# Kernel optimization log

Measured on AMD Instinct MI355X. Metric: run time of the kernel, lower is better.

## Reference

```python
import math
import jax, jax.numpy as jnp
import numpy as np

I_DIM = 64
N_MODES = 16
FACTOR = 4
EPS = 1e-5


def group_norm(x, w, b):
    # x: [B, M, N, C] channels-last; torch GroupNorm(C//16, C) over (group_channels, M, N)
    B, M, N, C = x.shape
    g = C // 16
    xr = x.reshape(B, M, N, g, C // g)
    mean = xr.mean(axis=(1, 2, 4), keepdims=True)
    var = xr.var(axis=(1, 2, 4), keepdims=True)
    xr = (xr - mean) * jax.lax.rsqrt(var + EPS)
    return xr.reshape(B, M, N, C) * w + b


def feed_forward(x, res, l1w, l1b, l2w, l2b, g1w, g1b, g2w, g2b, g3w, g3b):
    h = x @ l1w + l1b                      # [B,M,N,C*factor]
    h = group_norm(h, g1w, g1b)            # fork_1
    h = jax.nn.relu(h)
    h = h @ l2w + l2b                      # [B,M,N,C]
    h = group_norm(h, g2w, g2b)            # fork_2
    h = res + h
    h = group_norm(h, g3w, g3b)            # fork_3
    return h


def setup_inputs() -> dict:
    key = jax.random.key(0)
    ks = jax.random.split(key, 20)
    B, M, N, I = 4, 128, 128, I_DIM
    H = I * FACTOR
    z = jax.random.normal(ks[0], (B, 2 * M * N * I, 1), dtype=jnp.float32)
    x = jax.random.normal(ks[1], (B, M * N * I, 1), dtype=jnp.float32)
    # fourier weights [in, out, nm, nm, 2], xavier-ish scale
    fw_scale = math.sqrt(2.0 / (I + I))
    fw1 = jax.random.normal(ks[2], (I, I, N_MODES, N_MODES, 2), dtype=jnp.float32) * fw_scale
    fw2 = jax.random.normal(ks[3], (I, I, N_MODES, N_MODES, 2), dtype=jnp.float32) * fw_scale
    def ff_params(k0):
        kk = jax.random.split(k0, 4)
        return dict(
            l1w=jax.random.normal(kk[0], (I, H), dtype=jnp.float32) * math.sqrt(2.0 / (I + H)),
            l1b=jnp.zeros((H,), jnp.float32),
            l2w=jax.random.normal(kk[1], (H, I), dtype=jnp.float32) * math.sqrt(2.0 / (I + H)),
            l2b=jnp.zeros((I,), jnp.float32),
            g1w=jnp.ones((H,), jnp.float32), g1b=jnp.zeros((H,), jnp.float32),
            g2w=jnp.ones((I,), jnp.float32), g2b=jnp.zeros((I,), jnp.float32),
            g3w=jnp.ones((I,), jnp.float32), g3b=jnp.zeros((I,), jnp.float32),
        )
    bp = ff_params(ks[4])
    fp = ff_params(ks[5])
    out = {"z": z, "x": x, "fw1": fw1, "fw2": fw2}
    for name, p in (("b", bp), ("f", fp)):
        for k, v in p.items():
            out[f"{name}_{k}"] = v
    return out


def reference(z, x, fw1, fw2,
              b_l1w, b_l1b, b_l2w, b_l2b, b_g1w, b_g1b, b_g2w, b_g2b, b_g3w, b_g3b,
              f_l1w, f_l1b, f_l2w, f_l2b, f_g1w, f_g1b, f_g2w, f_g2b, f_g3w, f_g3b):
    I = I_DIM
    nm = N_MODES
    B = x.shape[0]
    M = N = int(math.sqrt(x.shape[1] // I))
    x4 = x.reshape(B, M, N, I)
    z5 = z.reshape(B, 2, M, N, I)
    backcast, forecast = z5[:, 0], z5[:, 1]
    x4 = x4 - backcast
    xc = jnp.transpose(x4, (0, 3, 1, 2))          # [B, I, M, N]
    x_ft = jnp.fft.rfft2(xc, s=(M, N), norm='ortho')  # [B, I, M, N//2+1] complex64
    w1 = fw1[..., 0] + 1j * fw1[..., 1]
    w2 = fw2[..., 0] + 1j * fw2[..., 1]
    top = jnp.einsum('bixy,ioxy->boxy', x_ft[:, :, :nm, :nm], w1)
    bot = jnp.einsum('bixy,ioxy->boxy', x_ft[:, :, -nm:, :nm], w2)
    out_ft = jnp.zeros((B, I, N, M // 2 + 1), dtype=x_ft.dtype)
    out_ft = out_ft.at[:, :, :nm, :nm].set(top).at[:, :, -nm:, :nm].set(bot)
    xo = jnp.fft.irfft2(out_ft, s=(N, M), norm='ortho')  # [B, I, M, N]
    xo = jnp.transpose(xo, (0, 2, 3, 1))                  # [B, M, N, I]
    backcast = feed_forward(xo, backcast, b_l1w, b_l1b, b_l2w, b_l2b,
                            b_g1w, b_g1b, b_g2w, b_g2b, b_g3w, b_g3b)
    forecast = feed_forward(xo, forecast, f_l1w, f_l1b, f_l2w, f_l2b,
                            f_g1w, f_g1b, f_g2w, f_g2b, f_g3w, f_g3b)
    out = jnp.stack([backcast, forecast], axis=1)         # [B, 2, M, N, I]
    return out.reshape(B, 2 * M * N * I, 1)
```

## Files before the change

kernel.cpp:

```cpp
#include <hip/hip_runtime.h>
#include <hip/hip_bf16.h>

typedef __hip_bfloat16 bf16;
typedef __attribute__((ext_vector_type(8))) short short8;
typedef __attribute__((ext_vector_type(4))) float f32x4;

#define PI2 6.283185307179586f
#define EPSV 1e-5f

__device__ __forceinline__ short f2bs(float f){
  bf16 h = __float2bfloat16(f);
  short s; __builtin_memcpy(&s, &h, 2); return s;
}
__device__ __forceinline__ float s2f(short s){
  bf16 h; __builtin_memcpy(&h, &s, 2); return __bfloat162float(h);
}
__device__ __forceinline__ float4 f4add(float4 a, float4 b){ return make_float4(a.x+b.x, a.y+b.y, a.z+b.z, a.w+b.w); }
__device__ __forceinline__ float4 f4sub(float4 a, float4 b){ return make_float4(a.x-b.x, a.y-b.y, a.z-b.z, a.w-b.w); }

__global__ __launch_bounds__(256) void k_prep(
    const float* __restrict__ fw1, const float* __restrict__ fw2,
    float2* __restrict__ FWT,
    const float* __restrict__ b_l1w, const float* __restrict__ b_l1b,
    const float* __restrict__ b_l2w, const float* __restrict__ b_l2b,
    const float* __restrict__ b_g1w, const float* __restrict__ b_g1b,
    const float* __restrict__ b_g2w, const float* __restrict__ b_g2b,
    const float* __restrict__ b_g3w, const float* __restrict__ b_g3b,
    const float* __restrict__ f_l1w, const float* __restrict__ f_l1b,
    const float* __restrict__ f_l2w, const float* __restrict__ f_l2b,
    const float* __restrict__ f_g1w, const float* __restrict__ f_g1b,
    const float* __restrict__ f_g2w, const float* __restrict__ f_g2b,
    const float* __restrict__ f_g3w, const float* __restrict__ f_g3b,
    short* __restrict__ W1g, short* __restrict__ W2g,
    float2* __restrict__ TWY, float2* __restrict__ TWX,
    float* __restrict__ PB, float* __restrict__ ST){
  __shared__ float Ls[16][512];
  int tid = threadIdx.x;
  if(blockIdx.x < 512){
    int arr = blockIdx.x >> 8, rem = blockIdx.x & 255;
    int i = rem >> 2, o0 = (rem & 3) * 16;
    const float* src = (arr ? fw2 : fw1) + ((size_t)(i*64 + o0))*512;
    for(int idx = tid; idx < 8192; idx += 256)
      Ls[idx >> 9][idx & 511] = src[idx];
    __syncthreads();
    int kxw = tid >> 4, ky = tid & 15;
    float2* dst = FWT + ((size_t)((arr*16 + kxw)*16 + ky))*4096 + i*64 + o0;
    for(int ol = 0; ol < 16; ol++)
      dst[ol] = make_float2(Ls[ol][tid*2], Ls[ol][tid*2 + 1]);
    return;
  }
  int i = (blockIdx.x - 512)*256 + tid;
  if(i < 32768){
    int br = i >> 14, r = i & 16383;
    int fid = r >> 9, lane = (r >> 3) & 63, e = r & 7;
    int hb = fid & 1, t = (fid >> 1) & 3, ch = fid >> 3;
    int l15 = lane & 15, quad = lane >> 4;
    int n = ch*64 + t*16 + l15;
    int k = hb*32 + quad*8 + e;
    const float* src = br ? f_l1w : b_l1w;
    W1g[i] = f2bs(src[k*256 + n]);
    return;
  }
  i -= 32768;
  if(i < 32768){
    int br = i >> 14, r = i & 16383;
    int fid = r >> 9, lane = (r >> 3) & 63, e = r & 7;
    int hb = fid & 1, t = (fid >> 1) & 3, ch = fid >> 3;
    int l15 = lane & 15, quad = lane >> 4;
    int n = t*16 + l15;
    int k = ch*64 + hb*32 + quad*8 + e;
    const float* src = br ? f_l2w : b_l2w;
    W2g[i] = f2bs(src[k*64 + n]);
    return;
  }
  i -= 32768;
  if(i < 2048){
    int ky = i >> 7, n = i & 127;
    float ang = PI2 * (float)((ky*n) & 127) / 128.0f;
    float s, c; sincosf(ang, &s, &c);
    TWY[i] = make_float2(c, s);
    return;
  }
  i -= 2048;
  if(i < 4096){
    int kp = i >> 7, m = i & 127;
    int kx = kp < 16 ? kp : 96 + kp;
    float ang = PI2 * (float)((kx*m) & 127) / 128.0f;
    float s, c; sincosf(ang, &s, &c);
    TWX[i] = make_float2(c, s);
    return;
  }
  i -= 4096;
  if(i < 384){ ST[i] = 0.f; return; }
  i -= 384;
  if(i < 2176){
    int br = i >= 1088; int o = i - br*1088;
    float* pb = PB + br*2048;
    float v;
    if(o < 256)       v = (br ? f_l1b : b_l1b)[o];
    else if(o < 512)  v = (br ? f_g1w : b_g1w)[o-256];
    else if(o < 768)  v = (br ? f_g1b : b_g1b)[o-512];
    else if(o < 832)  v = (br ? f_l2b : b_l2b)[o-768];
    else if(o < 896)  v = (br ? f_g2w : b_g2w)[o-832];
    else if(o < 960)  v = (br ? f_g2b : b_g2b)[o-896];
    else if(o < 1024) v = (br ? f_g3w : b_g3w)[o-960];
    else              v = (br ? f_g3b : b_g3b)[o-1024];
    pb[o] = v;
  }
}

__global__ __launch_bounds__(256) void k_ydft(const float* __restrict__ x,
                                              const float* __restrict__ z,
                                              const float2* __restrict__ TWY,
                                              float2* __restrict__ Y){
  __shared__ float P[32][64], Q[32][64], R[32][64], S[32][64];
  __shared__ float2 twl[16][32];
  int b = blockIdx.x >> 7, m = blockIdx.x & 127;
  int tid = threadIdx.x;
  const float4* xp = (const float4*)(x + ((size_t)(b*128 + m)*128)*64);
  const float4* zp = (const float4*)(z + ((size_t)((b*2 + 0)*128 + m)*128)*64);
  int i4 = tid & 15, n0 = tid >> 4;
  #pragma unroll
  for(int it = 0; it < 2; it++){
    int np = n0 + it*16;
    float4 ea = f4sub(xp[np*16 + i4],      zp[np*16 + i4]);
    float4 eb = f4sub(xp[(np+32)*16 + i4], zp[(np+32)*16 + i4]);
    float4 ec = f4sub(xp[(np+64)*16 + i4], zp[(np+64)*16 + i4]);
    float4 ed = f4sub(xp[(np+96)*16 + i4], zp[(np+96)*16 + i4]);
    float4 sum_ac = f4add(ea, ec), sum_bd = f4add(eb, ed);
    *(float4*)&P[np][i4*4] = f4add(sum_ac, sum_bd);
    *(float4*)&Q[np][i4*4] = f4sub(sum_ac, sum_bd);
    *(float4*)&R[np][i4*4] = f4sub(ea, ec);
    *(float4*)&S[np][i4*4] = f4sub(eb, ed);
  }
  for(int idx = tid; idx < 512; idx += 256)
    twl[idx >> 5][idx & 31] = TWY[(idx >> 5)*128 + (idx & 31)];
  __syncthreads();
  int i = tid & 63, kq = tid >> 6;
  float re[4] = {0,0,0,0}, im[4] = {0,0,0,0};
  for(int np = 0; np < 32; np++){
    float p = P[np][i], q = Q[np][i], r = R[np][i], s = S[np][i];
    float2 t0 = twl[kq*4 + 0][np];
    float2 t1 = twl[kq*4 + 1][np];
    float2 t2 = twl[kq*4 + 2][np];
    float2 t3 = twl[kq*4 + 3][np];
    re[0] += p*t0.x;            im[0] -= p*t0.y;
    re[1] += r*t1.x - s*t1.y;   im[1] -= s*t1.x + r*t1.y;
    re[2] += q*t2.x;            im[2] -= q*t2.y;
    re[3] += r*t3.x + s*t3.y;   im[3] += s*t3.x - r*t3.y;
  }
  #pragma unroll
  for(int j = 0; j < 4; j++)
    Y[((b*128 + m)*16 + kq*4 + j)*64 + i] = make_float2(re[j], im[j]);
}

__global__ __launch_bounds__(256) void k_xdft(const float2* __restrict__ Y,
                                              const float2* __restrict__ TWX,
                                              float2* __restrict__ X2){
  __shared__ float2 twl[16][64];
  __shared__ float sc[128][8];
  int bi = blockIdx.x;
  int b = bi >> 6, ky = (bi >> 2) & 15, half = (bi >> 1) & 1, ih = bi & 1;
  int tid = threadIdx.x;
  for(int idx = tid; idx < 1024; idx += 256)
    twl[idx >> 6][idx & 63] = TWX[(half*16 + (idx >> 6))*128 + (idx & 63)];
  __syncthreads();
  int i = ih*32 + (tid & 31), grp = (tid >> 5) & 3, mh2 = tid >> 7;
  const float2* yb = Y + (size_t)b*131072 + ky*64 + i;
  float re[4] = {0,0,0,0}, im[4] = {0,0,0,0};
  for(int mi = 0; mi < 32; mi++){
    int mp = mh2*32 + mi;
    float2 y1 = yb[(size_t)mp*1024];
    float2 y2 = yb[(size_t)(mp + 64)*1024];
    float2 ye = make_float2(y1.x + y2.x, y1.y + y2.y);
    float2 yo = make_float2(y1.x - y2.x, y1.y - y2.y);
    float2 t0 = twl[grp*4 + 0][mp];
    float2 t1 = twl[grp*4 + 1][mp];
    float2 t2 = twl[grp*4 + 2][mp];
    float2 t3 = twl[grp*4 + 3][mp];
    re[0] += ye.x*t0.x + ye.y*t0.y;  im[0] += ye.y*t0.x - ye.x*t0.y;
    re[1] += yo.x*t1.x + yo.y*t1.y;  im[1] += yo.y*t1.x - yo.x*t1.y;
    re[2] += ye.x*t2.x + ye.y*t2.y;  im[2] += ye.y*t2.x - ye.x*t2.y;
    re[3] += yo.x*t3.x + yo.y*t3.y;  im[3] += yo.y*t3.x - yo.x*t3.y;
  }
  if(mh2){
    int sl = tid & 127;
    #pragma unroll
    for(int j = 0; j < 4; j++){ sc[sl][j] = re[j]; sc[sl][4 + j] = im[j]; }
  }
  __syncthreads();
  if(!mh2){
    const float scn = 1.0f/128.0f;
    #pragma unroll
    for(int j = 0; j < 4; j++){
      float rr = (re[j] + sc[tid][j])*scn;
      float ii = (im[j] + sc[tid][4 + j])*scn;
      int kp = half*16 + grp*4 + j;
      X2[((b*32 + kp)*16 + ky)*64 + i] = make_float2(rr, ii);
    }
  }
}

__global__ __launch_bounds__(256) void k_mix(float2* __restrict__ X2,
                                             const float2* __restrict__ FWT){
  __shared__ float2 Xs[2][4][64];
  __shared__ float sc[2][64][8];
  int tid = threadIdx.x;
  for(int idx = tid; idx < 512; idx += 256){
    int pl = idx >> 8, b = (idx >> 6) & 3, i = idx & 63;
    int p = blockIdx.x*2 + pl; int kp = p >> 4, ky = p & 15;
    Xs[pl][b][i] = X2[((b*32 + kp)*16 + ky)*64 + i];
  }
  __syncthreads();
  int o = tid & 63, w = tid >> 6, pl = w >> 1, ih = w & 1;
  int p = blockIdx.x*2 + pl; int kp = p >> 4, ky = p & 15;
  int arr = kp < 16 ? 0 : 1, kxw = kp < 16 ? kp : kp - 16;
  const float2* wp = FWT + ((size_t)((arr*16 + kxw)*16 + ky))*4096;
  float rr[4] = {0,0,0,0}, ii[4] = {0,0,0,0};
  for(int i = ih*32; i < ih*32 + 32; i++){
    float2 wv = wp[i*64 + o];
    #pragma unroll
    for(int b = 0; b < 4; b++){
      float xr = Xs[pl][b][i].x, xi = Xs[pl][b][i].y;
      rr[b] += xr*wv.x - xi*wv.y;
      ii[b] += xr*wv.y + xi*wv.x;
    }
  }
  if(ih){
    #pragma unroll
    for(int b = 0; b < 4; b++){ sc[pl][o][b*2] = rr[b]; sc[pl][o][b*2 + 1] = ii[b]; }
  }
  __syncthreads();
  if(!ih){
    #pragma unroll
    for(int b = 0; b < 4; b++){
      float r2 = rr[b] + sc[pl][o][b*2], i2 = ii[b] + sc[pl][o][b*2 + 1];
      X2[((b*32 + kp)*16 + ky)*64 + o] = make_float2(r2, i2);
    }
  }
}

__global__ __launch_bounds__(256) void k_inv1(const float2* __restrict__ OF,
                                              const float2* __restrict__ TWX,
                                              float2* __restrict__ T){
  __shared__ float2 Fl[32][16];
  __shared__ float2 twl[32][64];
  int bi = blockIdx.x;
  int b = bi >> 6, ky = (bi >> 2) & 15, oq = bi & 3;
  int tid = threadIdx.x;
  for(int idx = tid; idx < 512; idx += 256){
    int kp = idx >> 4, ol = idx & 15;
    Fl[kp][ol] = OF[((b*32 + kp)*16 + ky)*64 + oq*16 + ol];
  }
  for(int idx = tid; idx < 2048; idx += 256){
    int kp = idx >> 6, ml = idx & 63;
    twl[kp][ml] = TWX[kp*128 + ml];
  }
  __syncthreads();
  int ol = tid & 15, mg = tid >> 4;
  float reE[4] = {0,0,0,0}, imE[4] = {0,0,0,0};
  float reO[4] = {0,0,0,0}, imO[4] = {0,0,0,0};
  for(int kp = 0; kp < 32; kp += 2){
    float2 fe = Fl[kp][ol], fo = Fl[kp + 1][ol];
    #pragma unroll
    for(int u = 0; u < 4; u++){
      float2 te = twl[kp][mg*4 + u], to = twl[kp + 1][mg*4 + u];
      reE[u] += fe.x*te.x - fe.y*te.y;
      imE[u] += fe.x*te.y + fe.y*te.x;
      reO[u] += fo.x*to.x - fo.y*to.y;
      imO[u] += fo.x*to.y + fo.y*to.x;
    }
  }
  int o = oq*16 + ol;
  #pragma unroll
  for(int u = 0; u < 4; u++){
    int ml = mg*4 + u;
    T[((b*128 + ml)*16 + ky)*64 + o]      = make_float2(reE[u] + reO[u], imE[u] + imO[u]);
    T[((b*128 + ml + 64)*16 + ky)*64 + o] = make_float2(reE[u] - reO[u], imE[u] - imO[u]);
  }
}

__global__ __launch_bounds__(256) void k_inv2(const float2* __restrict__ T,
                                              const float2* __restrict__ TWY,
                                              bf16* __restrict__ XO,
                                              float* __restrict__ CZ){
  __shared__ float2 twl[16][64];
  int b = blockIdx.x >> 6, mp = blockIdx.x & 63;
  int m0 = mp*2, m1 = m0 + 1;
  int tid = threadIdx.x;
  int flat = blockIdx.x*256 + tid;
  if(flat < 16640) CZ[flat] = 0.f;
  for(int idx = tid; idx < 1024; idx += 256)
    twl[idx >> 6][idx & 63] = TWY[(idx >> 6)*128 + (idx & 63)];
  int o = tid & 63, ng = tid >> 6;
  const float2* tp0 = T + ((size_t)(b*128 + m0)*16)*64 + o;
  const float2* tp1 = T + ((size_t)(b*128 + m1)*16)*64 + o;
  float t0a = tp0[0].x, t0b = tp1[0].x;
  float ax[15], ay[15], bx2[15], by2[15];
  #pragma unroll
  for(int u = 0; u < 15; u++){
    float2 v0 = tp0[(u + 1)*64]; ax[u]  = 2.f*v0.x; ay[u]  = 2.f*v0.y;
    float2 v1 = tp1[(u + 1)*64]; bx2[u] = 2.f*v1.x; by2[u] = 2.f*v1.y;
  }
  __syncthreads();
  const float scn = 1.0f/128.0f;
  bf16* xo0 = XO + ((size_t)(b*128 + m0)*128)*64 + o;
  bf16* xo1 = XO + ((size_t)(b*128 + m1)*128)*64 + o;
  for(int np = ng*16; np < ng*16 + 16; np++){
    float A0 = t0a, B0 = 0.f, A1 = t0b, B1 = 0.f;
    #pragma unroll
    for(int u = 0; u < 15; u++){
      float2 t = twl[u + 1][np];
      float pr0 = ax[u]*t.x  - ay[u]*t.y;
      float pr1 = bx2[u]*t.x - by2[u]*t.y;
      if(u & 1){ A0 += pr0; A1 += pr1; }
      else     { B0 += pr0; B1 += pr1; }
    }
    xo0[(size_t)np*64]        = __float2bfloat16((A0 + B0)*scn);
    xo0[(size_t)(np + 64)*64] = __float2bfloat16((A0 - B0)*scn);
    xo1[(size_t)np*64]        = __float2bfloat16((A1 + B1)*scn);
    xo1[(size_t)(np + 64)*64] = __float2bfloat16((A1 - B1)*scn);
  }
}

__global__ __launch_bounds__(256) void k_cov(const bf16* __restrict__ XO,
                                             float* __restrict__ Cg,
                                             float* __restrict__ SX){
  __shared__ short XT[64][264];
  __shared__ float sxl[64];
  int tid = threadIdx.x;
  int b = blockIdx.x >> 4, ck = blockIdx.x & 15;
  if(tid < 64) sxl[tid] = 0.f;
  float sxp[8];
  #pragma unroll
  for(int e = 0; e < 8; e++) sxp[e] = 0.f;
  int c0 = (tid & 7)*8;
  int lane = tid & 63, w = tid >> 6, l15 = lane & 15, quad = lane >> 4;
  f32x4 acc[4];
  #pragma unroll
  for(int tj = 0; tj < 4; tj++) acc[tj] = (f32x4){0.f,0.f,0.f,0.f};
  for(int st = 0; st < 4; st++){
    size_t pbase = (size_t)b*16384 + (size_t)ck*1024 + st*256;
    const short* xg = (const short*)XO + pbase*64;
    __syncthreads();
    for(int it = 0; it < 8; it++){
      int p = it*32 + (tid >> 3);
      short8 v = *(const short8*)(xg + (size_t)p*64 + c0);
      #pragma unroll
      for(int e = 0; e < 8; e++){
        XT[c0+e][p] = v[e];
        sxp[e] += s2f(v[e]);
      }
    }
    __syncthreads();
    for(int kk = 0; kk < 8; kk++){
      short8 a = *(const short8*)&XT[w*16 + l15][kk*32 + quad*8];
      #pragma unroll
      for(int tj = 0; tj < 4; tj++){
        short8 bfr = *(const short8*)&XT[tj*16 + l15][kk*32 + quad*8];
        acc[tj] = __builtin_amdgcn_mfma_f32_16x16x32_bf16(a, bfr, acc[tj], 0, 0, 0);
      }
    }
  }
  #pragma unroll
  for(int e = 0; e < 8; e++) atomicAdd(&sxl[c0+e], sxp[e]);
  __syncthreads();
  float* Cb = Cg + b*4096;
  #pragma unroll
  for(int tj = 0; tj < 4; tj++)
    #pragma unroll
    for(int r = 0; r < 4; r++)
      atomicAdd(&Cb[(w*16 + quad*4 + r)*64 + tj*16 + l15], acc[tj][r]);
  if(tid < 64) atomicAdd(&SX[b*64 + tid], sxl[tid]);
}

__global__ __launch_bounds__(256) void k_stat(const float* __restrict__ Cg,
                                              const float* __restrict__ SX,
                                              const short* __restrict__ W1g,
                                              const float* __restrict__ PB,
                                              float* __restrict__ ST){
  __shared__ float Cl[64][65];
  __shared__ float Wl[16][64];
  __shared__ float sxl[64];
  __shared__ float g2[2];
  int tid = threadIdx.x;
  int br = blockIdx.x >> 6, b = (blockIdx.x >> 4) & 3, g = blockIdx.x & 15;
  const float* Cb = Cg + b*4096;
  for(int u = tid; u < 4096; u += 256) Cl[u >> 6][u & 63] = Cb[u];
  const short* W1 = W1g + br*16384;
  for(int u = tid; u < 1024; u += 256){
    int nl = u >> 6, k = u & 63;
    int n = g*16 + nl;
    int fid = ((n >> 6)*4 + ((n >> 4) & 3))*2 + (k >> 5);
    int lane = ((k >> 3) & 3)*16 + (n & 15);
    Wl[nl][k] = s2f(W1[fid*512 + lane*8 + (k & 7)]);
  }
  if(tid < 64) sxl[tid] = SX[b*64 + tid];
  if(tid < 2) g2[tid] = 0.f;
  __syncthreads();
  int nl = tid >> 4, ic = tid & 15;
  float qa = 0.f, sa = 0.f;
  for(int io = 0; io < 4; io++){
    int i = ic*4 + io;
    float wi = Wl[nl][i];
    float dot = 0.f;
    #pragma unroll 8
    for(int j = 0; j < 64; j++) dot += Cl[i][j]*Wl[nl][j];
    qa += wi*dot;
    sa += wi*sxl[i];
  }
  for(int off = 8; off; off >>= 1){
    qa += __shfl_xor(qa, off);
    sa += __shfl_xor(sa, off);
  }
  if(ic == 0){
    float bn = PB[br*2048 + g*16 + nl];
    float hs = sa + 16384.f*bn;
    float hq = qa + 2.f*bn*sa + 16384.f*bn*bn;
    atomicAdd(&g2[0], hs); atomicAdd(&g2[1], hq);
  }
  __syncthreads();
  if(tid == 0){
    float* S1 = ST + br*192;
    S1[(b*16 + g)*2]     = g2[0];
    S1[(b*16 + g)*2 + 1] = g2[1];
  }
}

__global__ __launch_bounds__(256, 2) void k_ffmain(const bf16* __restrict__ XO,
                                                   const short* __restrict__ W1g,
                                                   const short* __restrict__ W2g,
                                                   const float* __restrict__ PB,
                                                   const float* __restrict__ ST,
                                                   const float* __restrict__ z,
                                                   float* __restrict__ CS,
                                                   float* __restrict__ out){
  __shared__ short Ws1[16384];
  __shared__ short Ws2[16384];
  __shared__ short Hn[64][72];
  __shared__ float mu1[16], rs1[16];
  __shared__ float cs[5][64];
  int tid = threadIdx.x;
  int br = blockIdx.x >> 8, rb = blockIdx.x & 255;
  int r0 = rb << 8, b = rb >> 6;
  const float* pb = PB + br*2048;
  {
    const uint4* g1 = (const uint4*)(W1g + br*16384);
    const uint4* g2w = (const uint4*)(W2g + br*16384);
    uint4* s1 = (uint4*)Ws1; uint4* s2 = (uint4*)Ws2;
    #pragma unroll
    for(int u = 0; u < 8; u++){
      s1[u*256 + tid] = g1[u*256 + tid];
      s2[u*256 + tid] = g2w[u*256 + tid];
    }
  }
  if(tid < 16){
    const float cnt = 262144.f;
    const float* S1 = ST + br*192;
    float s = S1[(b*16 + tid)*2], q = S1[(b*16 + tid)*2 + 1];
    float mean = s/cnt, var = q/cnt - mean*mean;
    mu1[tid] = mean; rs1[tid] = rsqrtf(fmaxf(var, 0.f) + EPSV);
  }
  {
    float* c1 = &cs[0][0];
    c1[tid] = 0.f;
    if(tid < 64) c1[256 + tid] = 0.f;
  }
  __syncthreads();
  int lane = tid & 63, w = tid >> 6, l15 = lane & 15, quad = lane >> 4;
  int myrow = w*16 + l15;
  float sh[4]  = {0,0,0,0}, sh2[4] = {0,0,0,0};
  float sz[4]  = {0,0,0,0}, sz2[4] = {0,0,0,0}, shz[4] = {0,0,0,0};
  for(int c = 0; c < 4; c++){
    const short* xop = (const short*)XO + ((size_t)(r0 + c*64 + myrow))*64;
    short8 a0 = *(const short8*)(xop + quad*8);
    short8 a1 = *(const short8*)(xop + 32 + quad*8);
    f32x4 acc2[4];
    #pragma unroll
    for(int t = 0; t < 4; t++) acc2[t] = (f32x4){0.f,0.f,0.f,0.f};
    for(int ch = 0; ch < 4; ch++){
      #pragma unroll
      for(int t = 0; t < 4; t++){
        int fid = (ch*4 + t)*2;
        short8 b0 = *(const short8*)(Ws1 + fid*512 + lane*8);
        short8 b1 = *(const short8*)(Ws1 + fid*512 + 512 + lane*8);
        f32x4 acc = {0.f,0.f,0.f,0.f};
        acc = __builtin_amdgcn_mfma_f32_16x16x32_bf16(a0, b0, acc, 0, 0, 0);
        acc = __builtin_amdgcn_mfma_f32_16x16x32_bf16(a1, b1, acc, 0, 0, 0);
        int n = ch*64 + t*16 + l15, gi = n >> 4;
        float w1v = pb[256 + n];
        float gwv = w1v * rs1[gi];
        float gbv = (pb[n] - mu1[gi])*rs1[gi]*w1v + pb[512 + n];
        #pragma unroll
        for(int r = 0; r < 4; r++){
          float hv = acc[r]*gwv + gbv;
          hv = hv > 0.f ? hv : 0.f;
          Hn[w*16 + quad*4 + r][t*16 + l15] = f2bs(hv);
        }
      }
      short8 ha0 = *(short8*)&Hn[myrow][quad*8];
      short8 ha1 = *(short8*)&Hn[myrow][32 + quad*8];
      #pragma unroll
      for(int t = 0; t < 4; t++){
        int fid = (ch*4 + t)*2;
        short8 b0 = *(const short8*)(Ws2 + fid*512 + lane*8);
        short8 b1 = *(const short8*)(Ws2 + fid*512 + 512 + lane*8);
        acc2[t] = __builtin_amdgcn_mfma_f32_16x16x32_bf16(ha0, b0, acc2[t], 0, 0, 0);
        acc2[t] = __builtin_amdgcn_mfma_f32_16x16x32_bf16(ha1, b1, acc2[t], 0, 0, 0);
      }
    }
    size_t obase_off = ((size_t)(b*2 + br)*16384 + (r0 & 16383) + c*64)*64;
    float* obase = out + obase_off;
    const float* zbase = z + obase_off;
    #pragma unroll
    for(int t = 0; t < 4; t++){
      int col = t*16 + l15;
      float bias2 = pb[768 + col];
      #pragma unroll
      for(int r = 0; r < 4; r++){
        size_t off = (size_t)(w*16 + quad*4 + r)*64 + col;
        float h2 = acc2[t][r] + bias2;
        float zv = zbase[off];
        obase[off] = h2;
        sh[t] += h2; sh2[t] += h2*h2;
        sz[t] += zv; sz2[t] += zv*zv; shz[t] += h2*zv;
      }
    }
  }
  #pragma unroll
  for(int t = 0; t < 4; t++){
    float v0 = sh[t], v1 = sh2[t], v2 = sz[t], v3 = sz2[t], v4 = shz[t];
    v0 += __shfl_xor(v0, 16); v0 += __shfl_xor(v0, 32);
    v1 += __shfl_xor(v1, 16); v1 += __shfl_xor(v1, 32);
    v2 += __shfl_xor(v2, 16); v2 += __shfl_xor(v2, 32);
    v3 += __shfl_xor(v3, 16); v3 += __shfl_xor(v3, 32);
    v4 += __shfl_xor(v4, 16); v4 += __shfl_xor(v4, 32);
    if(quad == 0){
      int ch = t*16 + l15;
      atomicAdd(&cs[0][ch], v0); atomicAdd(&cs[1][ch], v1);
      atomicAdd(&cs[2][ch], v2); atomicAdd(&cs[3][ch], v3);
      atomicAdd(&cs[4][ch], v4);
    }
  }
  __syncthreads();
  float* slab = CS + (size_t)blockIdx.x*320;
  const float* c1 = &cs[0][0];
  slab[tid] = c1[tid];
  if(tid < 64) slab[256 + tid] = c1[256 + tid];
}

__global__ __launch_bounds__(256) void k_statB(const float* __restrict__ CS,
                                               const float* __restrict__ PB,
                                               float* __restrict__ CF){
  __shared__ float chs[5][64];
  __shared__ float mu2s[4], rs2s[4], tg[4], tq[4], mu3s[4], rs3s[4];
  int br = blockIdx.x >> 2, b = blockIdx.x & 3;
  int tid = threadIdx.x;
  const float* base = CS + ((size_t)(br*256 + b*64))*320;
  float* c1 = &chs[0][0];
  for(int v = tid; v < 320; v += 256){
    float s = 0.f;
    for(int k = 0; k < 64; k++) s += base[(size_t)k*320 + v];
    c1[v] = s;
  }
  __syncthreads();
  if(tid < 4){
    float s = 0.f, q = 0.f;
    for(int o = tid*16; o < tid*16 + 16; o++){ s += chs[0][o]; q += chs[1][o]; }
    float mean = s/262144.f, var = q/262144.f - mean*mean;
    mu2s[tid] = mean; rs2s[tid] = rsqrtf(fmaxf(var, 0.f) + EPSV);
    tg[tid] = 0.f; tq[tid] = 0.f;
  }
  __syncthreads();
  const float* pb = PB + br*2048;
  if(tid < 64){
    int o = tid, g = o >> 4;
    float w2v = pb[832 + o], b2v = pb[896 + o];
    float gw = w2v*rs2s[g], gb = b2v - mu2s[g]*rs2s[g]*w2v;
    float Sh = chs[0][o], Sh2 = chs[1][o], Sz = chs[2][o], Sz2 = chs[3][o], Shz = chs[4][o];
    float st = gw*Sh + Sz + 16384.f*gb;
    float sq = gw*gw*Sh2 + Sz2 + 16384.f*gb*gb + 2.f*gw*Shz + 2.f*gw*gb*Sh + 2.f*gb*Sz;
    atomicAdd(&tg[g], st); atomicAdd(&tq[g], sq);
  }
  __syncthreads();
  if(tid < 4){
    float mean = tg[tid]/262144.f, var = tq[tid]/262144.f - mean*mean;
    mu3s[tid] = mean; rs3s[tid] = rsqrtf(fmaxf(var, 0.f) + EPSV);
  }
  __syncthreads();
  if(tid < 64){
    int o = tid, g = o >> 4;
    float w2v = pb[832 + o], b2v = pb[896 + o];
    float gw = w2v*rs2s[g], gb = b2v - mu2s[g]*rs2s[g]*w2v;
    float w3v = pb[960 + o], b3v = pb[1024 + o];
    float gw3 = w3v*rs3s[g], gb3 = b3v - mu3s[g]*rs3s[g]*w3v;
    float* cf = CF + (size_t)(br*4 + b)*192;
    cf[o]       = gw*gw3;
    cf[64 + o]  = gw3;
    cf[128 + o] = gb*gw3 + gb3;
  }
}

__global__ __launch_bounds__(256) void k_final(const float* __restrict__ z,
                                               const float* __restrict__ CF,
                                               float* __restrict__ out){
  int tid = blockIdx.x*256 + threadIdx.x;
  const float4* z4 = (const float4*)z;
  const float4* cf4 = (const float4*)CF;
  float4* o4 = (float4*)out;
  #pragma unroll
  for(int r = 0; r < 8; r++){
    int i4 = r*262144 + tid;
    int s = i4 >> 18;
    int b = s >> 1, br = s & 1;
    int cbase = (br*4 + b)*48 + (i4 & 15);
    float4 a = cf4[cbase], bb = cf4[cbase + 16], g = cf4[cbase + 32];
    float4 h = o4[i4], zv = z4[i4];
    o4[i4] = make_float4(h.x*a.x + zv.x*bb.x + g.x,
                         h.y*a.y + zv.y*bb.y + g.y,
                         h.z*a.z + zv.z*bb.z + g.z,
                         h.w*a.w + zv.w*bb.w + g.w);
  }
}

extern "C" void kernel_launch(void* const* d_in, const int* in_sizes, int n_in,
                              void* d_out, int out_size, void* d_ws, size_t ws_size,
                              hipStream_t stream){
  const float* z   = (const float*)d_in[0];
  const float* x   = (const float*)d_in[1];
  const float* fw1 = (const float*)d_in[2];
  const float* fw2 = (const float*)d_in[3];
  char* ws = (char*)d_ws;
  float2* Y   = (float2*)(ws + 0);
  float2* X2  = (float2*)(ws + 4194304);
  float2* T   = Y;
  bf16*   XO  = (bf16*)(ws + 5242880);
  float*  ST  = (float*)(ws + 13631488);
  short*  W1g = (short*)(ws + 13633536);
  short*  W2g = (short*)(ws + 13699072);
  float2* TWY = (float2*)(ws + 13764608);
  float2* TWX = (float2*)(ws + 13780992);
  float*  PB  = (float*)(ws + 13813760);
  float2* FWT = (float2*)(ws + 13830144);
  float*  Cg  = (float*)(ws + 13830144);
  float*  SX  = Cg + 16384;
  float*  CS  = (float*)(ws + 14878720);
  float*  CF  = (float*)(ws + 15927296);

  const float* p[20];
  for(int i = 0; i < 20; i++) p[i] = (const float*)d_in[4 + i];

  k_prep<<<802, 256, 0, stream>>>(fw1, fw2, FWT,
                                  p[0],p[1],p[2],p[3],p[4],p[5],p[6],p[7],p[8],p[9],
                                  p[10],p[11],p[12],p[13],p[14],p[15],p[16],p[17],p[18],p[19],
                                  W1g, W2g, TWY, TWX, PB, ST);
  k_ydft<<<512, 256, 0, stream>>>(x, z, TWY, Y);
  k_xdft<<<256, 256, 0, stream>>>(Y, TWX, X2);
  k_mix<<<256, 256, 0, stream>>>(X2, FWT);
  k_inv1<<<256, 256, 0, stream>>>(X2, TWX, T);
  k_inv2<<<256, 256, 0, stream>>>(T, TWY, XO, Cg);
  k_cov<<<64, 256, 0, stream>>>(XO, Cg, SX);
  k_stat<<<128, 256, 0, stream>>>(Cg, SX, W1g, PB, ST);
  k_ffmain<<<512, 256, 0, stream>>>(XO, W1g, W2g, PB, ST, z, CS, (float*)d_out);
  k_statB<<<8, 256, 0, stream>>>(CS, PB, CF);
  k_final<<<1024, 256, 0, stream>>>(z, CF, (float*)d_out);
}
```

Measured before the change: 261.7 us.

## Fuse prep with y-DFT and widen parallelism across the spectral kernels

Merges the weight-prep kernel with the y-direction DFT so there is one fewer launch, and the DFT computes its twiddles inline with sincosf while packing its shared tiles as float2/float4 pairs. xdft, mix and inv1 go to 512-thread blocks that split the reduction four or two ways and combine partial sums through shared memory. inv2 and cov launch twice as many blocks, each doing half the work. ffmain preloads its activation fragments and the z values into registers before the main loop. The aim is more parallelism in the small, latency-bound stages, at the cost of extra shared-memory reductions and higher register pressure.

```diff
diff --git a/kernel.cpp b/kernel.cpp
--- a/kernel.cpp
+++ b/kernel.cpp
@@ -18,7 +18,8 @@
 __device__ __forceinline__ float4 f4add(float4 a, float4 b){ return make_float4(a.x+b.x, a.y+b.y, a.z+b.z, a.w+b.w); }
 __device__ __forceinline__ float4 f4sub(float4 a, float4 b){ return make_float4(a.x-b.x, a.y-b.y, a.z-b.z, a.w-b.w); }
 
-__global__ __launch_bounds__(256) void k_prep(
+__global__ __launch_bounds__(256) void k_prep_ydft(
+    const float* __restrict__ x, const float* __restrict__ z,
     const float* __restrict__ fw1, const float* __restrict__ fw2,
     float2* __restrict__ FWT,
     const float* __restrict__ b_l1w, const float* __restrict__ b_l1b,
@@ -33,11 +34,64 @@
     const float* __restrict__ f_g3w, const float* __restrict__ f_g3b,
     short* __restrict__ W1g, short* __restrict__ W2g,
     float2* __restrict__ TWY, float2* __restrict__ TWX,
-    float* __restrict__ PB, float* __restrict__ ST){
-  __shared__ float Ls[16][512];
-  int tid = threadIdx.x;
-  if(blockIdx.x < 512){
-    int arr = blockIdx.x >> 8, rem = blockIdx.x & 255;
+    float* __restrict__ PB, float* __restrict__ ST,
+    float2* __restrict__ Y){
+  __shared__ __align__(16) char sm[36864];
+  int tid = threadIdx.x;
+  int bi = blockIdx.x;
+  if(bi < 512){
+    float2 (*PQ)[64] = (float2(*)[64])sm;
+    float2 (*RS)[64] = (float2(*)[64])(sm + 16384);
+    float4 (*twl)[32] = (float4(*)[32])(sm + 32768);
+    int b = bi >> 7, m = bi & 127;
+    const float4* xp = (const float4*)(x + ((size_t)(b*128 + m)*128)*64);
+    const float4* zp = (const float4*)(z + ((size_t)((b*2 + 0)*128 + m)*128)*64);
+    int i4 = tid & 15, n0 = tid >> 4;
+    #pragma unroll
+    for(int it = 0; it < 2; it++){
+      int np = n0 + it*16;
+      float4 ea = f4sub(xp[np*16 + i4],      zp[np*16 + i4]);
+      float4 eb = f4sub(xp[(np+32)*16 + i4], zp[(np+32)*16 + i4]);
+      float4 ec = f4sub(xp[(np+64)*16 + i4], zp[(np+64)*16 + i4]);
+      float4 ed = f4sub(xp[(np+96)*16 + i4], zp[(np+96)*16 + i4]);
+      float4 sac = f4add(ea, ec), sbd = f4add(eb, ed);
+      float4 P = f4add(sac, sbd), Q = f4sub(sac, sbd);
+      float4 R = f4sub(ea, ec),  S = f4sub(eb, ed);
+      *(float4*)&PQ[np][i4*4]     = make_float4(P.x, Q.x, P.y, Q.y);
+      *(float4*)&PQ[np][i4*4 + 2] = make_float4(P.z, Q.z, P.w, Q.w);
+      *(float4*)&RS[np][i4*4]     = make_float4(R.x, S.x, R.y, S.y);
+      *(float4*)&RS[np][i4*4 + 2] = make_float4(R.z, S.z, R.w, S.w);
+    }
+    {
+      int kq2 = tid >> 5, np = tid & 31;
+      int ky0 = (kq2 >> 1)*4 + (kq2 & 1)*2;
+      float s0, c0, s1, c1;
+      sincosf(PI2*(float)((ky0*np) & 127)/128.f, &s0, &c0);
+      sincosf(PI2*(float)(((ky0+1)*np) & 127)/128.f, &s1, &c1);
+      twl[kq2][np] = make_float4(c0, s0, c1, s1);
+    }
+    __syncthreads();
+    int i = tid & 63, kq = tid >> 6;
+    float re[4] = {0,0,0,0}, im[4] = {0,0,0,0};
+    for(int np = 0; np < 32; np++){
+      float2 pq = PQ[np][i];
+      float2 rs = RS[np][i];
+      float4 t01 = twl[kq*2][np];
+      float4 t23 = twl[kq*2 + 1][np];
+      re[0] += pq.x*t01.x;               im[0] -= pq.x*t01.y;
+      re[1] += rs.x*t01.z - rs.y*t01.w;  im[1] -= rs.y*t01.z + rs.x*t01.w;
+      re[2] += pq.y*t23.x;               im[2] -= pq.y*t23.y;
+      re[3] += rs.x*t23.z + rs.y*t23.w;  im[3] += rs.y*t23.z - rs.x*t23.w;
+    }
+    #pragma unroll
+    for(int j = 0; j < 4; j++)
+      Y[((b*128 + m)*16 + kq*4 + j)*64 + i] = make_float2(re[j], im[j]);
+    return;
+  }
+  if(bi < 1024){
+    float (*Ls)[512] = (float(*)[512])sm;
+    int bb = bi - 512;
+    int arr = bb >> 8, rem = bb & 255;
     int i = rem >> 2, o0 = (rem & 3) * 16;
     const float* src = (arr ? fw2 : fw1) + ((size_t)(i*64 + o0))*512;
     for(int idx = tid; idx < 8192; idx += 256)
@@ -49,7 +103,7 @@
       dst[ol] = make_float2(Ls[ol][tid*2], Ls[ol][tid*2 + 1]);
     return;
   }
-  int i = (blockIdx.x - 512)*256 + tid;
+  int i = (bi - 1024)*256 + tid;
   if(i < 32768){
     int br = i >> 14, r = i & 16383;
     int fid = r >> 9, lane = (r >> 3) & 63, e = r & 7;
@@ -109,67 +163,22 @@
   }
 }
 
-__global__ __launch_bounds__(256) void k_ydft(const float* __restrict__ x,
-                                              const float* __restrict__ z,
-                                              const float2* __restrict__ TWY,
-                                              float2* __restrict__ Y){
-  __shared__ float P[32][64], Q[32][64], R[32][64], S[32][64];
-  __shared__ float2 twl[16][32];
-  int b = blockIdx.x >> 7, m = blockIdx.x & 127;
-  int tid = threadIdx.x;
-  const float4* xp = (const float4*)(x + ((size_t)(b*128 + m)*128)*64);
-  const float4* zp = (const float4*)(z + ((size_t)((b*2 + 0)*128 + m)*128)*64);
-  int i4 = tid & 15, n0 = tid >> 4;
-  #pragma unroll
-  for(int it = 0; it < 2; it++){
-    int np = n0 + it*16;
-    float4 ea = f4sub(xp[np*16 + i4],      zp[np*16 + i4]);
-    float4 eb = f4sub(xp[(np+32)*16 + i4], zp[(np+32)*16 + i4]);
-    float4 ec = f4sub(xp[(np+64)*16 + i4], zp[(np+64)*16 + i4]);
-    float4 ed = f4sub(xp[(np+96)*16 + i4], zp[(np+96)*16 + i4]);
-    float4 sum_ac = f4add(ea, ec), sum_bd = f4add(eb, ed);
-    *(float4*)&P[np][i4*4] = f4add(sum_ac, sum_bd);
-    *(float4*)&Q[np][i4*4] = f4sub(sum_ac, sum_bd);
-    *(float4*)&R[np][i4*4] = f4sub(ea, ec);
-    *(float4*)&S[np][i4*4] = f4sub(eb, ed);
-  }
-  for(int idx = tid; idx < 512; idx += 256)
-    twl[idx >> 5][idx & 31] = TWY[(idx >> 5)*128 + (idx & 31)];
-  __syncthreads();
-  int i = tid & 63, kq = tid >> 6;
-  float re[4] = {0,0,0,0}, im[4] = {0,0,0,0};
-  for(int np = 0; np < 32; np++){
-    float p = P[np][i], q = Q[np][i], r = R[np][i], s = S[np][i];
-    float2 t0 = twl[kq*4 + 0][np];
-    float2 t1 = twl[kq*4 + 1][np];
-    float2 t2 = twl[kq*4 + 2][np];
-    float2 t3 = twl[kq*4 + 3][np];
-    re[0] += p*t0.x;            im[0] -= p*t0.y;
-    re[1] += r*t1.x - s*t1.y;   im[1] -= s*t1.x + r*t1.y;
-    re[2] += q*t2.x;            im[2] -= q*t2.y;
-    re[3] += r*t3.x + s*t3.y;   im[3] += s*t3.x - r*t3.y;
-  }
-  #pragma unroll
-  for(int j = 0; j < 4; j++)
-    Y[((b*128 + m)*16 + kq*4 + j)*64 + i] = make_float2(re[j], im[j]);
-}
-
-__global__ __launch_bounds__(256) void k_xdft(const float2* __restrict__ Y,
+__global__ __launch_bounds__(512) void k_xdft(const float2* __restrict__ Y,
                                               const float2* __restrict__ TWX,
                                               float2* __restrict__ X2){
   __shared__ float2 twl[16][64];
-  __shared__ float sc[128][8];
+  __shared__ float sc[3][128][8];
   int bi = blockIdx.x;
   int b = bi >> 6, ky = (bi >> 2) & 15, half = (bi >> 1) & 1, ih = bi & 1;
   int tid = threadIdx.x;
-  for(int idx = tid; idx < 1024; idx += 256)
+  for(int idx = tid; idx < 1024; idx += 512)
     twl[idx >> 6][idx & 63] = TWX[(half*16 + (idx >> 6))*128 + (idx & 63)];
   __syncthreads();
-  int i = ih*32 + (tid & 31), grp = (tid >> 5) & 3, mh2 = tid >> 7;
+  int i = ih*32 + (tid & 31), grp = (tid >> 5) & 3, mq = tid >> 7;
   const float2* yb = Y + (size_t)b*131072 + ky*64 + i;
   float re[4] = {0,0,0,0}, im[4] = {0,0,0,0};
-  for(int mi = 0; mi < 32; mi++){
-    int mp = mh2*32 + mi;
+  for(int mi = 0; mi < 16; mi++){
+    int mp = mq*16 + mi;
     float2 y1 = yb[(size_t)mp*1024];
     float2 y2 = yb[(size_t)(mp + 64)*1024];
     float2 ye = make_float2(y1.x + y2.x, y1.y + y2.y);
@@ -183,41 +192,41 @@
     re[2] += ye.x*t2.x + ye.y*t2.y;  im[2] += ye.y*t2.x - ye.x*t2.y;
     re[3] += yo.x*t3.x + yo.y*t3.y;  im[3] += yo.y*t3.x - yo.x*t3.y;
   }
-  if(mh2){
+  if(mq){
     int sl = tid & 127;
     #pragma unroll
-    for(int j = 0; j < 4; j++){ sc[sl][j] = re[j]; sc[sl][4 + j] = im[j]; }
-  }
-  __syncthreads();
-  if(!mh2){
+    for(int j = 0; j < 4; j++){ sc[mq-1][sl][j] = re[j]; sc[mq-1][sl][4 + j] = im[j]; }
+  }
+  __syncthreads();
+  if(!mq){
     const float scn = 1.0f/128.0f;
     #pragma unroll
     for(int j = 0; j < 4; j++){
-      float rr = (re[j] + sc[tid][j])*scn;
-      float ii = (im[j] + sc[tid][4 + j])*scn;
+      float rr = (re[j] + sc[0][tid][j] + sc[1][tid][j] + sc[2][tid][j])*scn;
+      float ii = (im[j] + sc[0][tid][4+j] + sc[1][tid][4+j] + sc[2][tid][4+j])*scn;
       int kp = half*16 + grp*4 + j;
       X2[((b*32 + kp)*16 + ky)*64 + i] = make_float2(rr, ii);
     }
   }
 }
 
-__global__ __launch_bounds__(256) void k_mix(float2* __restrict__ X2,
+__global__ __launch_bounds__(512) void k_mix(float2* __restrict__ X2,
                                              const float2* __restrict__ FWT){
   __shared__ float2 Xs[2][4][64];
-  __shared__ float sc[2][64][8];
-  int tid = threadIdx.x;
-  for(int idx = tid; idx < 512; idx += 256){
-    int pl = idx >> 8, b = (idx >> 6) & 3, i = idx & 63;
-    int p = blockIdx.x*2 + pl; int kp = p >> 4, ky = p & 15;
-    Xs[pl][b][i] = X2[((b*32 + kp)*16 + ky)*64 + i];
-  }
-  __syncthreads();
-  int o = tid & 63, w = tid >> 6, pl = w >> 1, ih = w & 1;
+  __shared__ float sc[3][2][64][8];
+  int tid = threadIdx.x;
+  {
+    int pl = tid >> 8, bq = (tid >> 6) & 3, ii = tid & 63;
+    int p = blockIdx.x*2 + pl; int kp = p >> 4, kyy = p & 15;
+    Xs[pl][bq][ii] = X2[((bq*32 + kp)*16 + kyy)*64 + ii];
+  }
+  __syncthreads();
+  int o = tid & 63, w = tid >> 6, pl = w >> 2, iq = w & 3;
   int p = blockIdx.x*2 + pl; int kp = p >> 4, ky = p & 15;
   int arr = kp < 16 ? 0 : 1, kxw = kp < 16 ? kp : kp - 16;
   const float2* wp = FWT + ((size_t)((arr*16 + kxw)*16 + ky))*4096;
   float rr[4] = {0,0,0,0}, ii[4] = {0,0,0,0};
-  for(int i = ih*32; i < ih*32 + 32; i++){
+  for(int i = iq*16; i < iq*16 + 16; i++){
     float2 wv = wp[i*64 + o];
     #pragma unroll
     for(int b = 0; b < 4; b++){
@@ -226,41 +235,44 @@
       ii[b] += xr*wv.y + xi*wv.x;
     }
   }
-  if(ih){
-    #pragma unroll
-    for(int b = 0; b < 4; b++){ sc[pl][o][b*2] = rr[b]; sc[pl][o][b*2 + 1] = ii[b]; }
-  }
-  __syncthreads();
-  if(!ih){
+  if(iq){
+    #pragma unroll
+    for(int b = 0; b < 4; b++){ sc[iq-1][pl][o][b*2] = rr[b]; sc[iq-1][pl][o][b*2 + 1] = ii[b]; }
+  }
+  __syncthreads();
+  if(!iq){
     #pragma unroll
     for(int b = 0; b < 4; b++){
-      float r2 = rr[b] + sc[pl][o][b*2], i2 = ii[b] + sc[pl][o][b*2 + 1];
+      float r2 = rr[b] + sc[0][pl][o][b*2] + sc[1][pl][o][b*2] + sc[2][pl][o][b*2];
+      float i2 = ii[b] + sc[0][pl][o][b*2+1] + sc[1][pl][o][b*2+1] + sc[2][pl][o][b*2+1];
       X2[((b*32 + kp)*16 + ky)*64 + o] = make_float2(r2, i2);
     }
   }
 }
 
-__global__ __launch_bounds__(256) void k_inv1(const float2* __restrict__ OF,
+__global__ __launch_bounds__(512) void k_inv1(const float2* __restrict__ OF,
                                               const float2* __restrict__ TWX,
                                               float2* __restrict__ T){
   __shared__ float2 Fl[32][16];
   __shared__ float2 twl[32][64];
+  __shared__ float sc[256][16];
   int bi = blockIdx.x;
   int b = bi >> 6, ky = (bi >> 2) & 15, oq = bi & 3;
   int tid = threadIdx.x;
-  for(int idx = tid; idx < 512; idx += 256){
-    int kp = idx >> 4, ol = idx & 15;
+  {
+    int kp = tid >> 4, ol = tid & 15;
     Fl[kp][ol] = OF[((b*32 + kp)*16 + ky)*64 + oq*16 + ol];
   }
-  for(int idx = tid; idx < 2048; idx += 256){
+  for(int idx = tid; idx < 2048; idx += 512){
     int kp = idx >> 6, ml = idx & 63;
     twl[kp][ml] = TWX[kp*128 + ml];
   }
   __syncthreads();
-  int ol = tid & 15, mg = tid >> 4;
+  int ol = tid & 15, mg = (tid >> 4) & 15, kh = tid >> 8;
   float reE[4] = {0,0,0,0}, imE[4] = {0,0,0,0};
   float reO[4] = {0,0,0,0}, imO[4] = {0,0,0,0};
-  for(int kp = 0; kp < 32; kp += 2){
+  for(int ip = 0; ip < 8; ip++){
+    int kp = kh*16 + ip*2;
     float2 fe = Fl[kp][ol], fo = Fl[kp + 1][ol];
     #pragma unroll
     for(int u = 0; u < 4; u++){
@@ -271,12 +283,25 @@
       imO[u] += fo.x*to.y + fo.y*to.x;
     }
   }
-  int o = oq*16 + ol;
-  #pragma unroll
-  for(int u = 0; u < 4; u++){
-    int ml = mg*4 + u;
-    T[((b*128 + ml)*16 + ky)*64 + o]      = make_float2(reE[u] + reO[u], imE[u] + imO[u]);
-    T[((b*128 + ml + 64)*16 + ky)*64 + o] = make_float2(reE[u] - reO[u], imE[u] - imO[u]);
+  if(kh){
+    int sl = tid & 255;
+    #pragma unroll
+    for(int u = 0; u < 4; u++){
+      sc[sl][u] = reE[u]; sc[sl][4 + u] = imE[u];
+      sc[sl][8 + u] = reO[u]; sc[sl][12 + u] = imO[u];
+    }
+  }
+  __syncthreads();
+  if(!kh){
+    int o = oq*16 + ol;
+    #pragma unroll
+    for(int u = 0; u < 4; u++){
+      float rE = reE[u] + sc[tid][u],     iE = imE[u] + sc[tid][4 + u];
+      float rO = reO[u] + sc[tid][8 + u], iO = imO[u] + sc[tid][12 + u];
+      int ml = mg*4 + u;
+      T[((b*128 + ml)*16 + ky)*64 + o]      = make_float2(rE + rO, iE + iO);
+      T[((b*128 + ml + 64)*16 + ky)*64 + o] = make_float2(rE - rO, iE - iO);
+    }
   }
 }
 
@@ -285,41 +310,35 @@
                                               bf16* __restrict__ XO,
                                               float* __restrict__ CZ){
   __shared__ float2 twl[16][64];
-  int b = blockIdx.x >> 6, mp = blockIdx.x & 63;
-  int m0 = mp*2, m1 = m0 + 1;
-  int tid = threadIdx.x;
-  int flat = blockIdx.x*256 + tid;
+  int bi = blockIdx.x;
+  int b = bi >> 7, m = bi & 127;
+  int tid = threadIdx.x;
+  int flat = bi*256 + tid;
   if(flat < 16640) CZ[flat] = 0.f;
   for(int idx = tid; idx < 1024; idx += 256)
     twl[idx >> 6][idx & 63] = TWY[(idx >> 6)*128 + (idx & 63)];
   int o = tid & 63, ng = tid >> 6;
-  const float2* tp0 = T + ((size_t)(b*128 + m0)*16)*64 + o;
-  const float2* tp1 = T + ((size_t)(b*128 + m1)*16)*64 + o;
-  float t0a = tp0[0].x, t0b = tp1[0].x;
-  float ax[15], ay[15], bx2[15], by2[15];
+  const float2* tp = T + ((size_t)(b*128 + m)*16)*64 + o;
+  float t0a = tp[0].x;
+  float ax[15], ay[15];
   #pragma unroll
   for(int u = 0; u < 15; u++){
-    float2 v0 = tp0[(u + 1)*64]; ax[u]  = 2.f*v0.x; ay[u]  = 2.f*v0.y;
-    float2 v1 = tp1[(u + 1)*64]; bx2[u] = 2.f*v1.x; by2[u] = 2.f*v1.y;
+    float2 v = tp[(u + 1)*64];
+    ax[u] = 2.f*v.x; ay[u] = 2.f*v.y;
   }
   __syncthreads();
   const float scn = 1.0f/128.0f;
-  bf16* xo0 = XO + ((size_t)(b*128 + m0)*128)*64 + o;
-  bf16* xo1 = XO + ((size_t)(b*128 + m1)*128)*64 + o;
+  bf16* xo = XO + ((size_t)(b*128 + m)*128)*64 + o;
   for(int np = ng*16; np < ng*16 + 16; np++){
-    float A0 = t0a, B0 = 0.f, A1 = t0b, B1 = 0.f;
+    float A = t0a, B = 0.f;
     #pragma unroll
     for(int u = 0; u < 15; u++){
       float2 t = twl[u + 1][np];
-      float pr0 = ax[u]*t.x  - ay[u]*t.y;
-      float pr1 = bx2[u]*t.x - by2[u]*t.y;
-      if(u & 1){ A0 += pr0; A1 += pr1; }
-      else     { B0 += pr0; B1 += pr1; }
-    }
-    xo0[(size_t)np*64]        = __float2bfloat16((A0 + B0)*scn);
-    xo0[(size_t)(np + 64)*64] = __float2bfloat16((A0 - B0)*scn);
-    xo1[(size_t)np*64]        = __float2bfloat16((A1 + B1)*scn);
-    xo1[(size_t)(np + 64)*64] = __float2bfloat16((A1 - B1)*scn);
+      float pr = ax[u]*t.x - ay[u]*t.y;
+      if(u & 1) A += pr; else B += pr;
+    }
+    xo[(size_t)np*64]        = __float2bfloat16((A + B)*scn);
+    xo[(size_t)(np + 64)*64] = __float2bfloat16((A - B)*scn);
   }
 }
 
@@ -329,7 +348,7 @@
   __shared__ short XT[64][264];
   __shared__ float sxl[64];
   int tid = threadIdx.x;
-  int b = blockIdx.x >> 4, ck = blockIdx.x & 15;
+  int b = blockIdx.x >> 5, ck = blockIdx.x & 31;
   if(tid < 64) sxl[tid] = 0.f;
   float sxp[8];
   #pragma unroll
@@ -339,8 +358,8 @@
   f32x4 acc[4];
   #pragma unroll
   for(int tj = 0; tj < 4; tj++) acc[tj] = (f32x4){0.f,0.f,0.f,0.f};
-  for(int st = 0; st < 4; st++){
-    size_t pbase = (size_t)b*16384 + (size_t)ck*1024 + st*256;
+  for(int st = 0; st < 2; st++){
+    size_t pbase = (size_t)b*16384 + (size_t)ck*512 + st*256;
     const short* xg = (const short*)XO + pbase*64;
     __syncthreads();
     for(int it = 0; it < 8; it++){
@@ -444,6 +463,15 @@
   int br = blockIdx.x >> 8, rb = blockIdx.x & 255;
   int r0 = rb << 8, b = rb >> 6;
   const float* pb = PB + br*2048;
+  int lane = tid & 63, w = tid >> 6, l15 = lane & 15, quad = lane >> 4;
+  int myrow = w*16 + l15;
+  short8 a0r[4], a1r[4];
+  #pragma unroll
+  for(int c = 0; c < 4; c++){
+    const short* xop = (const short*)XO + ((size_t)(r0 + c*64 + myrow))*64;
+    a0r[c] = *(const short8*)(xop + quad*8);
+    a1r[c] = *(const short8*)(xop + 32 + quad*8);
+  }
   {
     const uint4* g1 = (const uint4*)(W1g + br*16384);
     const uint4* g2w = (const uint4*)(W2g + br*16384);
@@ -467,14 +495,18 @@
     if(tid < 64) c1[256 + tid] = 0.f;
   }
   __syncthreads();
-  int lane = tid & 63, w = tid >> 6, l15 = lane & 15, quad = lane >> 4;
-  int myrow = w*16 + l15;
   float sh[4]  = {0,0,0,0}, sh2[4] = {0,0,0,0};
   float sz[4]  = {0,0,0,0}, sz2[4] = {0,0,0,0}, shz[4] = {0,0,0,0};
+  #pragma unroll
   for(int c = 0; c < 4; c++){
-    const short* xop = (const short*)XO + ((size_t)(r0 + c*64 + myrow))*64;
-    short8 a0 = *(const short8*)(xop + quad*8);
-    short8 a1 = *(const short8*)(xop + 32 + quad*8);
+    size_t obase_off = ((size_t)(b*2 + br)*16384 + (r0 & 16383) + c*64)*64;
+    const float* zbase = z + obase_off;
+    float zr[16];
+    #pragma unroll
+    for(int t = 0; t < 4; t++)
+      #pragma unroll
+      for(int r = 0; r < 4; r++)
+        zr[t*4 + r] = zbase[(size_t)(w*16 + quad*4 + r)*64 + t*16 + l15];
     f32x4 acc2[4];
     #pragma unroll
     for(int t = 0; t < 4; t++) acc2[t] = (f32x4){0.f,0.f,0.f,0.f};
@@ -485,8 +517,8 @@
         short8 b0 = *(const short8*)(Ws1 + fid*512 + lane*8);
         short8 b1 = *(const short8*)(Ws1 + fid*512 + 512 + lane*8);
         f32x4 acc = {0.f,0.f,0.f,0.f};
-        acc = __builtin_amdgcn_mfma_f32_16x16x32_bf16(a0, b0, acc, 0, 0, 0);
-        acc = __builtin_amdgcn_mfma_f32_16x16x32_bf16(a1, b1, acc, 0, 0, 0);
+        acc = __builtin_amdgcn_mfma_f32_16x16x32_bf16(a0r[c], b0, acc, 0, 0, 0);
+        acc = __builtin_amdgcn_mfma_f32_16x16x32_bf16(a1r[c], b1, acc, 0, 0, 0);
         int n = ch*64 + t*16 + l15, gi = n >> 4;
         float w1v = pb[256 + n];
         float gwv = w1v * rs1[gi];
@@ -509,9 +541,7 @@
         acc2[t] = __builtin_amdgcn_mfma_f32_16x16x32_bf16(ha1, b1, acc2[t], 0, 0, 0);
       }
     }
-    size_t obase_off = ((size_t)(b*2 + br)*16384 + (r0 & 16383) + c*64)*64;
     float* obase = out + obase_off;
-    const float* zbase = z + obase_off;
     #pragma unroll
     for(int t = 0; t < 4; t++){
       int col = t*16 + l15;
@@ -520,7 +550,7 @@
       for(int r = 0; r < 4; r++){
         size_t off = (size_t)(w*16 + quad*4 + r)*64 + col;
         float h2 = acc2[t][r] + bias2;
-        float zv = zbase[off];
+        float zv = zr[t*4 + r];
         obase[off] = h2;
         sh[t] += h2; sh2[t] += h2*h2;
         sz[t] += zv; sz2[t] += zv*zv; shz[t] += h2*zv;
@@ -650,16 +680,15 @@
   const float* p[20];
   for(int i = 0; i < 20; i++) p[i] = (const float*)d_in[4 + i];
 
-  k_prep<<<802, 256, 0, stream>>>(fw1, fw2, FWT,
+  k_prep_ydft<<<1314, 256, 0, stream>>>(x, z, fw1, fw2, FWT,
                                   p[0],p[1],p[2],p[3],p[4],p[5],p[6],p[7],p[8],p[9],
                                   p[10],p[11],p[12],p[13],p[14],p[15],p[16],p[17],p[18],p[19],
-                                  W1g, W2g, TWY, TWX, PB, ST);
-  k_ydft<<<512, 256, 0, stream>>>(x, z, TWY, Y);
-  k_xdft<<<256, 256, 0, stream>>>(Y, TWX, X2);
-  k_mix<<<256, 256, 0, stream>>>(X2, FWT);
-  k_inv1<<<256, 256, 0, stream>>>(X2, TWX, T);
-  k_inv2<<<256, 256, 0, stream>>>(T, TWY, XO, Cg);
-  k_cov<<<64, 256, 0, stream>>>(XO, Cg, SX);
+                                  W1g, W2g, TWY, TWX, PB, ST, Y);
+  k_xdft<<<256, 512, 0, stream>>>(Y, TWX, X2);
+  k_mix<<<256, 512, 0, stream>>>(X2, FWT);
+  k_inv1<<<256, 512, 0, stream>>>(X2, TWX, T);
+  k_inv2<<<512, 256, 0, stream>>>(T, TWY, XO, Cg);
+  k_cov<<<128, 256, 0, stream>>>(XO, Cg, SX);
   k_stat<<<128, 256, 0, stream>>>(Cg, SX, W1g, PB, ST);
   k_ffmain<<<512, 256, 0, stream>>>(XO, W1g, W2g, PB, ST, z, CS, (float*)d_out);
   k_statB<<<8, 256, 0, stream>>>(CS, PB, CF);
```

Result: faster. 247.3 us (-5.5%).
